# Kernel optimization log

Measured on AMD Instinct MI355X. Metric: run time of the kernel, lower is better.

## Reference

```python
import jax, jax.numpy as jnp
import numpy as np

DIM, HEADS, NB_FEATURES = 512, 8, 64
HEAD_DIM = DIM // HEADS


def setup_inputs() -> dict:
    key = jax.random.key(0)
    k_x, k_qkv, k_pm, k_wp, k_bp = jax.random.split(key, 5)
    B, N = 8, 4096
    x = jax.random.normal(k_x, (B, N, DIM), dtype=jnp.float32)
    # to_qkv: Linear(dim, 3*dim, bias=False) -> apply as x @ w_qkv
    w_qkv = jax.random.normal(k_qkv, (DIM, 3 * DIM), dtype=jnp.float32) * (1.0 / np.sqrt(DIM))
    # random projection buffer [H, D, F]
    proj_mat = jax.random.normal(k_pm, (HEADS, HEAD_DIM, NB_FEATURES), dtype=jnp.float32)
    # output projection Linear(dim, dim) with bias
    w_proj = jax.random.normal(k_wp, (DIM, DIM), dtype=jnp.float32) * (1.0 / np.sqrt(DIM))
    b_proj = jax.random.normal(k_bp, (DIM,), dtype=jnp.float32) * 0.01
    return {"x": x, "w_qkv": w_qkv, "proj_mat": proj_mat, "w_proj": w_proj, "b_proj": b_proj}


def _phi(t, proj_mat):
    # t: [B,N,H,D], proj_mat: [H,D,F] -> [B,N,H,F]
    return jax.nn.elu(jnp.einsum('bnhd,hdf->bnhf', t, proj_mat)) + 1.0


def reference(x, w_qkv, proj_mat, w_proj, b_proj):
    B, N, dim = x.shape
    H, D = HEADS, dim // HEADS
    qkv = x @ w_qkv  # [B,N,3*dim]
    q, k, v = jnp.split(qkv, 3, axis=-1)
    q = q.reshape(B, N, H, D)
    k = k.reshape(B, N, H, D)
    v = v.reshape(B, N, H, D)
    q_phi = _phi(q, proj_mat)  # [B,N,H,F]
    k_phi = _phi(k, proj_mat)  # [B,N,H,F]
    kv = jnp.einsum('bnhf,bnhd->bhfd', k_phi, v)  # [B,H,F,D]
    z = 1.0 / jnp.einsum('bnhf,bhf->bnh', q_phi, k_phi.sum(axis=1))  # [B,N,H]
    out = jnp.einsum('bnhf,bhfd,bnh->bnhd', q_phi, kv, z)  # [B,N,H,D]
    out = out.reshape(B, N, H * D)
    return out @ w_proj + b_proj
```

## Files before the change

### kernel.cpp

```cpp
#include <hip/hip_runtime.h>
#include <hip/hip_bf16.h>

typedef __bf16 bf16_t;
typedef __bf16 bf16x4 __attribute__((ext_vector_type(4)));
typedef __bf16 bf16x8 __attribute__((ext_vector_type(8)));
typedef float f32x4 __attribute__((ext_vector_type(4)));

__device__ __forceinline__ void gload16(const void* g, void* l) {
  __builtin_amdgcn_global_load_lds((const __attribute__((address_space(1))) void*)g,
                                   (__attribute__((address_space(3))) void*)l, 16, 0, 0);
}

#define VMW(n) asm volatile("s_waitcnt vmcnt(" #n ")" ::: "memory")

__global__ __launch_bounds__(256) void prep_qk(const float* __restrict__ w_qkv,
                                               const float* __restrict__ proj,
                                               bf16_t* __restrict__ WeffT) {
  const int half = blockIdx.x >> 3, h = blockIdx.x & 7;
  const int i0 = blockIdx.y * 64;
  __shared__ float P[64 * 64];
  __shared__ float Wt[64][65];
  const int t = threadIdx.x;
  #pragma unroll
  for (int r = 0; r < 16; ++r) P[t + 256 * r] = proj[(size_t)h * 4096 + t + 256 * r];
  #pragma unroll
  for (int r = 0; r < 16; ++r) {
    const int idx = t + 256 * r;
    Wt[idx >> 6][idx & 63] =
        w_qkv[(size_t)(i0 + (idx >> 6)) * 1536 + half * 512 + h * 64 + (idx & 63)];
  }
  __syncthreads();
  const int i = t & 63, fg = t >> 6;
  for (int f = fg; f < 64; f += 4) {
    float s = 0.f;
    #pragma unroll
    for (int d = 0; d < 64; ++d) s += Wt[i][d] * P[d * 64 + f];
    WeffT[(size_t)(half * 512 + h * 64 + f) * 512 + i0 + i] = (bf16_t)s;
  }
}

__global__ __launch_bounds__(256) void prep_v(const float* __restrict__ w_qkv,
                                              bf16_t* __restrict__ WeffT) {
  __shared__ bf16_t tile[32][33];
  const int i0 = blockIdx.x * 32, n0 = blockIdx.y * 32;
  const int tn = threadIdx.x & 31, ti = threadIdx.x >> 5;
  #pragma unroll
  for (int p = 0; p < 4; ++p) {
    const int i = ti + p * 8;
    tile[i][tn] = (bf16_t)w_qkv[(size_t)(i0 + i) * 1536 + 1024 + n0 + tn];
  }
  __syncthreads();
  #pragma unroll
  for (int p = 0; p < 4; ++p) {
    const int n = ti + p * 8;
    WeffT[(size_t)(1024 + n0 + n) * 512 + i0 + tn] = tile[tn][n];
  }
}

__global__ __launch_bounds__(256) void cast_x(const f32x4* __restrict__ x,
                                              bf16x4* __restrict__ xb, int n4) {
  int i = blockIdx.x * 256 + threadIdx.x;
  if (i < n4) {
    f32x4 v = x[i];
    bf16x4 o;
    #pragma unroll
    for (int j = 0; j < 4; ++j) o[j] = (bf16_t)v[j];
    xb[i] = o;
  }
}

__global__ __launch_bounds__(512, 2) void gemm_qkv8(const bf16_t* __restrict__ x_bf,
                                                    const bf16_t* __restrict__ WeffT,
                                                    bf16_t* __restrict__ q_phi,
                                                    bf16_t* __restrict__ kT,
                                                    bf16_t* __restrict__ vT) {
  __shared__ alignas(16) char smem[131072];
  const int t = threadIdx.x;
  const int wid = t >> 6, l = t & 63;
  const int wr = wid >> 2, wc = wid & 3;
  const int lrow = l & 15, lkb = l >> 4;
  const int hw = blockIdx.x;
  const int bid = (hw & 7) * 96 + (hw >> 3);
  const int tb = bid / 6, fb = bid % 6;
  const size_t tok0 = (size_t)tb * 256;
  const int f0 = fb * 256;
  const bf16_t* Ap = x_bf + tok0 * 512;
  const bf16_t* Bp = WeffT + (size_t)f0 * 512;

  const int sr = t >> 2, su = t & 3;
  const int f_sr = (sr >> 1) & 3;
  const size_t a_off0 = (size_t)sr * 512 + ((su ^ f_sr) * 8);
  const size_t a_off1 = (size_t)(sr + 128) * 512 + ((su ^ f_sr) * 8);

  auto stageA = [&](int s) {
    char* dst = smem + (s & 3) * 16384;
    gload16(Ap + a_off0 + s * 32, dst + t * 16);
    gload16(Ap + a_off1 + s * 32, dst + 8192 + t * 16);
  };
  auto stageB = [&](int s) {
    char* dst = smem + 65536 + (s & 3) * 16384;
    gload16(Bp + a_off0 + s * 32, dst + t * 16);
    gload16(Bp + a_off1 + s * 32, dst + 8192 + t * 16);
  };

  int woff[8], xoff[4];
  #pragma unroll
  for (int m = 0; m < 8; ++m) {
    const int r = wr * 128 + m * 16 + lrow;
    woff[m] = r * 64 + ((lkb ^ ((r >> 1) & 3)) << 4);
  }
  #pragma unroll
  for (int n = 0; n < 4; ++n) {
    const int r = wc * 64 + n * 16 + lrow;
    xoff[n] = r * 64 + ((lkb ^ ((r >> 1) & 3)) << 4);
  }

  f32x4 acc[8][4];
  #pragma unroll
  for (int m = 0; m < 8; ++m)
    #pragma unroll
    for (int n = 0; n < 4; ++n) acc[m][n] = f32x4{0.f, 0.f, 0.f, 0.f};

  stageA(0); stageB(0); stageA(1); stageB(1); stageA(2); stageB(2);
  VMW(8);
  __builtin_amdgcn_s_barrier();

  #pragma unroll
  for (int kt = 0; kt < 16; ++kt) {
    const char* Xs = smem + (kt & 3) * 16384;
    const char* Ws = smem + 65536 + (kt & 3) * 16384;
    bf16x8 wf[4], xf[4];
    #pragma unroll
    for (int m = 0; m < 4; ++m) wf[m] = *(const bf16x8*)(Ws + woff[m]);
    #pragma unroll
    for (int n = 0; n < 4; ++n) xf[n] = *(const bf16x8*)(Xs + xoff[n]);
    if (kt + 3 < 16) stageA(kt + 3);
    __builtin_amdgcn_s_setprio(1);
    #pragma unroll
    for (int m = 0; m < 4; ++m)
      #pragma unroll
      for (int n = 0; n < 4; ++n)
        acc[m][n] = __builtin_amdgcn_mfma_f32_16x16x32_bf16(wf[m], xf[n], acc[m][n], 0, 0, 0);
    __builtin_amdgcn_s_setprio(0);
    #pragma unroll
    for (int m = 0; m < 4; ++m) wf[m] = *(const bf16x8*)(Ws + woff[4 + m]);
    if (kt + 3 < 16) stageB(kt + 3);
    __builtin_amdgcn_s_setprio(1);
    #pragma unroll
    for (int m = 0; m < 4; ++m)
      #pragma unroll
      for (int n = 0; n < 4; ++n)
        acc[4 + m][n] = __builtin_amdgcn_mfma_f32_16x16x32_bf16(wf[m], xf[n], acc[4 + m][n], 0, 0, 0);
    __builtin_amdgcn_s_setprio(0);
    if (kt <= 12) { VMW(8); } else if (kt == 13) { VMW(4); } else if (kt == 14) { VMW(0); }
    __builtin_amdgcn_s_barrier();
  }

  const bool doElu = (fb < 4);
  #pragma unroll
  for (int m = 0; m < 8; ++m) {
    const int feat = wr * 128 + m * 16 + lkb * 4;
    const int ub = feat >> 3, bo = (feat & 7) * 2;
    #pragma unroll
    for (int n = 0; n < 4; ++n) {
      const int trow = wc * 64 + n * 16 + lrow;
      bf16x4 o;
      #pragma unroll
      for (int j = 0; j < 4; ++j) {
        float v = acc[m][n][j];
        if (doElu) v = v > 0.f ? v + 1.f : __expf(v);
        o[j] = (bf16_t)v;
      }
      const int s = (trow ^ (trow >> 3)) & 7;
      *(bf16x4*)(smem + trow * 512 + ((ub ^ s) << 4) + bo) = o;
    }
  }
  __syncthreads();
  if (fb < 2) {
    #pragma unroll
    for (int p = 0; p < 16; ++p) {
      const int flat = p * 512 + t;
      const int trow = flat >> 5, u = flat & 31;
      const int s = (trow ^ (trow >> 3)) & 7;
      bf16x8 vv = *(const bf16x8*)(smem + trow * 512 + ((u ^ s) << 4));
      *(bf16x8*)&q_phi[(tok0 + trow) * 512 + f0 + u * 8] = vv;
    }
  } else {
    const int b = (int)(tok0 >> 12);
    const int nn0 = (int)(tok0 & 4095);
    bf16_t* base = (fb < 4) ? (kT + ((size_t)(b * 512 + (fb - 2) * 256)) * 4096)
                            : (vT + ((size_t)(b * 512 + (fb - 4) * 256)) * 4096);
    #pragma unroll
    for (int p = 0; p < 16; ++p) {
      const int fl = (p & 7) * 32 + (t >> 4);
      const int tg = (p >> 3) * 16 + (t & 15);
      const int ub = fl >> 3, bo = (fl & 7) * 2;
      bf16x8 vv;
      #pragma unroll
      for (int j = 0; j < 8; ++j) {
        const int tok = tg * 8 + j;
        const int s = (tok ^ (tok >> 3)) & 7;
        vv[j] = *(const bf16_t*)(smem + tok * 512 + ((ub ^ s) << 4) + bo);
      }
      *(bf16x8*)(base + (size_t)fl * 4096 + nn0 + tg * 8) = vv;
    }
  }
}

__global__ __launch_bounds__(256) void kv_mfma(const bf16_t* __restrict__ kT,
                                               const bf16_t* __restrict__ vT,
                                               float* __restrict__ kv,
                                               float* __restrict__ ksum) {
  const int bh = blockIdx.x;
  const int nbase = blockIdx.y * 512;
  __shared__ alignas(16) char smem[32768];
  const int t = threadIdx.x, w = t >> 6, l = t & 63;
  const int wr = w >> 1, wc = w & 1;
  const int lrow = l & 15, lkb = l >> 4;
  const int st_r = l >> 3;
  const int st_c = ((l & 7) ^ st_r) * 8;
  const bf16_t* Kp = kT + (size_t)bh * 64 * 4096;
  const bf16_t* Vp = vT + (size_t)bh * 64 * 4096;

  f32x4 acc[2][2];
  #pragma unroll
  for (int m = 0; m < 2; ++m)
    #pragma unroll
    for (int n = 0; n < 2; ++n) acc[m][n] = f32x4{0.f, 0.f, 0.f, 0.f};
  float ksf[2] = {0.f, 0.f};

  #pragma unroll
  for (int c = 0; c < 2; ++c) {
    const int q8 = w * 2 + c;
    gload16(Kp + (size_t)(q8 * 8 + st_r) * 4096 + nbase + st_c, smem + q8 * 1024);
    gload16(Vp + (size_t)(q8 * 8 + st_r) * 4096 + nbase + st_c, smem + 8192 + q8 * 1024);
  }
  __syncthreads();

  int cur = 0;
  for (int st = 0; st < 8; ++st) {
    if (st < 7) {
      char* nb = smem + (cur ^ 1) * 16384;
      const int nb2 = nbase + (st + 1) * 64;
      #pragma unroll
      for (int c = 0; c < 2; ++c) {
        const int q8 = w * 2 + c;
        gload16(Kp + (size_t)(q8 * 8 + st_r) * 4096 + nb2 + st_c, nb + q8 * 1024);
        gload16(Vp + (size_t)(q8 * 8 + st_r) * 4096 + nb2 + st_c, nb + 8192 + q8 * 1024);
      }
    }
    const char* KsB = smem + cur * 16384;
    const char* VsB = KsB + 8192;
    bf16x8 af[2][2], bf[2][2];
    #pragma unroll
    for (int m = 0; m < 2; ++m) {
      const int r = wr * 32 + m * 16 + lrow;
      #pragma unroll
      for (int kk = 0; kk < 2; ++kk) {
        const int kb = lkb + kk * 4;
        af[m][kk] = *(const bf16x8*)(KsB + r * 128 + (((kb ^ (r & 7)) & 7) << 4));
      }
    }
    #pragma unroll
    for (int n = 0; n < 2; ++n) {
      const int r = wc * 32 + n * 16 + lrow;
      #pragma unroll
      for (int kk = 0; kk < 2; ++kk) {
        const int kb = lkb + kk * 4;
        bf[n][kk] = *(const bf16x8*)(VsB + r * 128 + (((kb ^ (r & 7)) & 7) << 4));
      }
    }
    #pragma unroll
    for (int m = 0; m < 2; ++m)
      #pragma unroll
      for (int n = 0; n < 2; ++n) {
        acc[m][n] = __builtin_amdgcn_mfma_f32_16x16x32_bf16(af[m][0], bf[n][0], acc[m][n], 0, 0, 0);
        acc[m][n] = __builtin_amdgcn_mfma_f32_16x16x32_bf16(af[m][1], bf[n][1], acc[m][n], 0, 0, 0);
      }
    if (wc == 0) {
      #pragma unroll
      for (int m = 0; m < 2; ++m)
        #pragma unroll
        for (int kk = 0; kk < 2; ++kk)
          #pragma unroll
          for (int j = 0; j < 8; ++j) ksf[m] += (float)af[m][kk][j];
    }
    __syncthreads();
    cur ^= 1;
  }

  float* kvp = kv + (size_t)bh * 4096;
  #pragma unroll
  for (int m = 0; m < 2; ++m)
    #pragma unroll
    for (int n = 0; n < 2; ++n)
      #pragma unroll
      for (int j = 0; j < 4; ++j)
        atomicAdd(&kvp[(wr * 32 + m * 16 + lkb * 4 + j) * 64 + wc * 32 + n * 16 + lrow],
                  acc[m][n][j]);
  if (wc == 0) {
    #pragma unroll
    for (int m = 0; m < 2; ++m) {
      float s = ksf[m];
      s += __shfl_xor(s, 16);
      s += __shfl_xor(s, 32);
      if (l < 16) atomicAdd(&ksum[(size_t)bh * 64 + wr * 32 + m * 16 + l], s);
    }
  }
}

__global__ __launch_bounds__(256) void w2_kernel(const float* __restrict__ kv,
                                                 const float* __restrict__ w_proj,
                                                 bf16_t* __restrict__ W2T) {
  const int bh = blockIdx.x, b = bh >> 3, h = bh & 7;
  const int j0 = blockIdx.y * 64;
  const int t = threadIdx.x;
  __shared__ float kvs[64][64];
  __shared__ float wps[64][64];
  const float* kvp = kv + (size_t)bh * 4096;
  #pragma unroll
  for (int i = 0; i < 16; ++i) ((float*)kvs)[t + 256 * i] = kvp[t + 256 * i];
  {
    const int d = t >> 2, c16 = (t & 3) * 16;
    const float* src = w_proj + (size_t)(h * 64 + d) * 512 + j0 + c16;
    #pragma unroll
    for (int j = 0; j < 16; ++j) wps[d][c16 + j] = src[j];
  }
  __syncthreads();
  const int fq = t >> 4, jq = t & 15;
  float acc[4][4] = {};
  for (int d = 0; d < 64; ++d) {
    float kf[4], wj[4];
    #pragma unroll
    for (int i = 0; i < 4; ++i) kf[i] = kvs[fq * 4 + i][d];
    #pragma unroll
    for (int i = 0; i < 4; ++i) wj[i] = wps[d][jq * 4 + i];
    #pragma unroll
    for (int i = 0; i < 4; ++i)
      #pragma unroll
      for (int j = 0; j < 4; ++j) acc[i][j] += kf[i] * wj[j];
  }
  #pragma unroll
  for (int j = 0; j < 4; ++j)
    #pragma unroll
    for (int i = 0; i < 4; ++i)
      W2T[((size_t)b * 512 + j0 + jq * 4 + j) * 512 + h * 64 + fq * 4 + i] = (bf16_t)acc[i][j];
}

__global__ __launch_bounds__(256) void zq_kernel(const bf16_t* __restrict__ qphi,
                                                 const float* __restrict__ ksum,
                                                 bf16_t* __restrict__ zq) {
  const int row = blockIdx.x * 4 + (threadIdx.x >> 6);
  const int l = threadIdx.x & 63;
  const int b = row >> 12;
  const int h = l >> 3, f8 = (l & 7) * 8;
  const bf16_t* src = qphi + (size_t)row * 512 + h * 64 + f8;
  bf16x8 v = *(const bf16x8*)src;
  const float* ks = ksum + ((size_t)b * 8 + h) * 64 + f8;
  float part = 0.f;
  float vf[8];
  #pragma unroll
  for (int j = 0; j < 8; ++j) { vf[j] = (float)v[j]; part += vf[j] * ks[j]; }
  part += __shfl_xor(part, 1);
  part += __shfl_xor(part, 2);
  part += __shfl_xor(part, 4);
  const float z = 1.f / part;
  bf16x8 o;
  #pragma unroll
  for (int j = 0; j < 8; ++j) o[j] = (bf16_t)(vf[j] * z);
  *(bf16x8*)(zq + (size_t)row * 512 + h * 64 + f8) = o;
}

__global__ __launch_bounds__(256) void gemm_out(const bf16_t* __restrict__ W2T,
                                                const bf16_t* __restrict__ zq,
                                                float* __restrict__ Cout,
                                                const float* __restrict__ bias) {
  constexpr int K = 512, BK = 64;
  __shared__ alignas(16) char smem[65536];
  const int t = threadIdx.x, w = t >> 6, l = t & 63;
  const int hw = blockIdx.x;
  const int bid = (hw & 7) * 128 + (hw >> 3);
  const int z = bid >> 7;
  const int rem = bid & 127;
  const int qblk = rem >> 2, pblk = rem & 3;
  const size_t tok0 = (size_t)qblk * 128;
  const int pj0 = pblk * 128;
  const bf16_t* Pp = W2T + ((size_t)z * 512 + pj0) * 512;
  const bf16_t* Qp = zq + ((size_t)z * 4096 + tok0) * 512;

  const int wr = w >> 1, wc = w & 1;
  const int lrow = l & 15, lkb = l >> 4;
  const int st_r = l >> 3;
  const int st_c = ((l & 7) ^ st_r) * 8;

  f32x4 acc[4][4];
  #pragma unroll
  for (int m = 0; m < 4; ++m)
    #pragma unroll
    for (int n = 0; n < 4; ++n) acc[m][n] = f32x4{0.f, 0.f, 0.f, 0.f};

  #pragma unroll
  for (int c = 0; c < 4; ++c) {
    const int q8 = c * 4 + w;
    gload16(Pp + (size_t)(q8 * 8 + st_r) * K + st_c, smem + q8 * 1024);
    gload16(Qp + (size_t)(q8 * 8 + st_r) * K + st_c, smem + 16384 + q8 * 1024);
  }
  __syncthreads();

  int cur = 0;
  for (int kt = 0; kt < K; kt += BK) {
    if (kt + BK < K) {
      char* nb = smem + (cur ^ 1) * 32768;
      #pragma unroll
      for (int c = 0; c < 4; ++c) {
        const int q8 = c * 4 + w;
        gload16(Pp + (size_t)(q8 * 8 + st_r) * K + kt + BK + st_c, nb + q8 * 1024);
        gload16(Qp + (size_t)(q8 * 8 + st_r) * K + kt + BK + st_c, nb + 16384 + q8 * 1024);
      }
    }
    const char* PsB = smem + cur * 32768;
    const char* QsB = PsB + 16384;
    bf16x8 pf[4][2], qf[4][2];
    #pragma unroll
    for (int m = 0; m < 4; ++m) {
      const int r = wr * 64 + m * 16 + lrow;
      #pragma unroll
      for (int kk = 0; kk < 2; ++kk) {
        const int kb = lkb + kk * 4;
        pf[m][kk] = *(const bf16x8*)(PsB + r * 128 + (((kb ^ (r & 7)) & 7) << 4));
      }
    }
    #pragma unroll
    for (int n = 0; n < 4; ++n) {
      const int r = wc * 64 + n * 16 + lrow;
      #pragma unroll
      for (int kk = 0; kk < 2; ++kk) {
        const int kb = lkb + kk * 4;
        qf[n][kk] = *(const bf16x8*)(QsB + r * 128 + (((kb ^ (r & 7)) & 7) << 4));
      }
    }
    #pragma unroll
    for (int m = 0; m < 4; ++m)
      #pragma unroll
      for (int n = 0; n < 4; ++n) {
        acc[m][n] = __builtin_amdgcn_mfma_f32_16x16x32_bf16(pf[m][0], qf[n][0], acc[m][n], 0, 0, 0);
        acc[m][n] = __builtin_amdgcn_mfma_f32_16x16x32_bf16(pf[m][1], qf[n][1], acc[m][n], 0, 0, 0);
      }
    __syncthreads();
    cur ^= 1;
  }

  float* ep = (float*)smem;
  #pragma unroll
  for (int p = 0; p < 2; ++p) {
    if (p) __syncthreads();
    #pragma unroll
    for (int nn2 = 0; nn2 < 2; ++nn2) {
      const int n = p * 2 + nn2;
      const int r6 = wc * 32 + (n & 1) * 16 + lrow;
      #pragma unroll
      for (int m = 0; m < 4; ++m) {
        const int pr0 = wr * 64 + m * 16 + lkb * 4;
        f32x4 v = acc[m][n];
        const f32x4 bv = *(const f32x4*)&bias[pj0 + pr0];
        #pragma unroll
        for (int j = 0; j < 4; ++j) v[j] += bv[j];
        const int u = pr0 >> 2;
        *(f32x4*)((char*)ep + r6 * 512 + ((u ^ (r6 & 31)) << 4)) = v;
      }
    }
    __syncthreads();
    #pragma unroll
    for (int i = 0; i < 8; ++i) {
      const int flat = i * 256 + t;
      const int r6 = flat >> 5, u2 = flat & 31;
      f32x4 v = *(const f32x4*)((char*)ep + r6 * 512 + ((u2 ^ (r6 & 31)) << 4));
      const int qc = (r6 >> 5) * 64 + p * 32 + (r6 & 31);
      *(f32x4*)&Cout[((size_t)z * 4096 + tok0 + qc) * 512 + pj0 + u2 * 4] = v;
    }
  }
}

extern "C" void kernel_launch(void* const* d_in, const int* in_sizes, int n_in,
                              void* d_out, int out_size, void* d_ws, size_t ws_size,
                              hipStream_t stream) {
  const float* x      = (const float*)d_in[0];
  const float* w_qkv  = (const float*)d_in[1];
  const float* proj   = (const float*)d_in[2];
  const float* w_proj = (const float*)d_in[3];
  const float* b_proj = (const float*)d_in[4];
  float* out = (float*)d_out;
  char* ws = (char*)d_ws;

  bf16_t* x_bf  = (bf16_t*)(ws + 0);
  bf16_t* WeffT = (bf16_t*)(ws + 33554432);
  bf16_t* q_phi = (bf16_t*)(ws + 35127296);
  bf16_t* kT    = (bf16_t*)(ws + 68681728);
  bf16_t* vT    = (bf16_t*)(ws + 102236160);
  float*  kv    = (float*)(ws + 135790592);
  float*  ksum  = (float*)(ws + 136839168);
  bf16_t* W2T   = (bf16_t*)(ws + 136855552);
  bf16_t* zq    = (bf16_t*)(ws + 141049856);

  prep_qk<<<dim3(16, 8), 256, 0, stream>>>(w_qkv, proj, WeffT);
  prep_v<<<dim3(16, 16), 256, 0, stream>>>(w_qkv, WeffT);
  cast_x<<<16384, 256, 0, stream>>>((const f32x4*)x, (bf16x4*)x_bf, 4194304);
  gemm_qkv8<<<768, 512, 0, stream>>>(x_bf, WeffT, q_phi, kT, vT);
  hipMemsetAsync(kv, 0, 1048576 + 16384, stream);
  kv_mfma<<<dim3(64, 8), 256, 0, stream>>>(kT, vT, kv, ksum);
  w2_kernel<<<dim3(64, 8), 256, 0, stream>>>(kv, w_proj, W2T);
  zq_kernel<<<8192, 256, 0, stream>>>(q_phi, ksum, zq);
  gemm_out<<<1024, 256, 0, stream>>>(W2T, zq, out, b_proj);
}
```

Baseline: 184.8 us.

## Fuse x cast into QKV GEMM and z-normalization into output GEMM

Removes the standalone cast_x and zq_kernel launches. The QKV GEMM now reads fp32 x directly, converting it to bf16 in registers before writing to LDS. The output GEMM loads q_phi, computes the per-head normalizer from ksum held in LDS, and writes the scaled bf16 tile into LDS itself. This drops the intermediate x_bf and zq round-trips through HBM. In exchange, the A-operand pipeline shrinks to register prefetch with double buffering, B uses triple buffering, LDS drops to 80KB, and the epilogue is split into two halves.

```diff
diff --git a/kernel.cpp b/kernel.cpp
--- a/kernel.cpp
+++ b/kernel.cpp
@@ -4,6 +4,7 @@
 typedef __bf16 bf16_t;
 typedef __bf16 bf16x4 __attribute__((ext_vector_type(4)));
 typedef __bf16 bf16x8 __attribute__((ext_vector_type(8)));
+typedef float f32x2 __attribute__((ext_vector_type(2)));
 typedef float f32x4 __attribute__((ext_vector_type(4)));
 
 __device__ __forceinline__ void gload16(const void* g, void* l) {
@@ -12,6 +13,7 @@
 }
 
 #define VMW(n) asm volatile("s_waitcnt vmcnt(" #n ")" ::: "memory")
+#define LGKM0() asm volatile("s_waitcnt lgkmcnt(0)" ::: "memory")
 
 __global__ __launch_bounds__(256) void prep_qk(const float* __restrict__ w_qkv,
                                                const float* __restrict__ proj,
@@ -57,24 +59,12 @@
   }
 }
 
-__global__ __launch_bounds__(256) void cast_x(const f32x4* __restrict__ x,
-                                              bf16x4* __restrict__ xb, int n4) {
-  int i = blockIdx.x * 256 + threadIdx.x;
-  if (i < n4) {
-    f32x4 v = x[i];
-    bf16x4 o;
-    #pragma unroll
-    for (int j = 0; j < 4; ++j) o[j] = (bf16_t)v[j];
-    xb[i] = o;
-  }
-}
-
-__global__ __launch_bounds__(512, 2) void gemm_qkv8(const bf16_t* __restrict__ x_bf,
+__global__ __launch_bounds__(512, 2) void gemm_qkv8(const float* __restrict__ x,
                                                     const bf16_t* __restrict__ WeffT,
                                                     bf16_t* __restrict__ q_phi,
                                                     bf16_t* __restrict__ kT,
                                                     bf16_t* __restrict__ vT) {
-  __shared__ alignas(16) char smem[131072];
+  __shared__ alignas(16) char smem[81920];
   const int t = threadIdx.x;
   const int wid = t >> 6, l = t & 63;
   const int wr = wid >> 2, wc = wid & 3;
@@ -84,23 +74,37 @@
   const int tb = bid / 6, fb = bid % 6;
   const size_t tok0 = (size_t)tb * 256;
   const int f0 = fb * 256;
-  const bf16_t* Ap = x_bf + tok0 * 512;
+  const float* Ap = x + tok0 * 512;
   const bf16_t* Bp = WeffT + (size_t)f0 * 512;
 
   const int sr = t >> 2, su = t & 3;
   const int f_sr = (sr >> 1) & 3;
-  const size_t a_off0 = (size_t)sr * 512 + ((su ^ f_sr) * 8);
-  const size_t a_off1 = (size_t)(sr + 128) * 512 + ((su ^ f_sr) * 8);
-
-  auto stageA = [&](int s) {
-    char* dst = smem + (s & 3) * 16384;
-    gload16(Ap + a_off0 + s * 32, dst + t * 16);
-    gload16(Ap + a_off1 + s * 32, dst + 8192 + t * 16);
+  const int scol = (su ^ f_sr) * 8;
+
+  f32x4 areg[4];
+  auto loadA = [&](int s) {
+    const float* p0 = Ap + (size_t)sr * 512 + scol + s * 32;
+    const float* p1 = Ap + (size_t)(sr + 128) * 512 + scol + s * 32;
+    areg[0] = *(const f32x4*)p0;
+    areg[1] = *(const f32x4*)(p0 + 4);
+    areg[2] = *(const f32x4*)p1;
+    areg[3] = *(const f32x4*)(p1 + 4);
+  };
+  auto writeA = [&](int s) {
+    char* dst = smem + (s & 1) * 16384;
+    bf16x8 o0, o1;
+    #pragma unroll
+    for (int j = 0; j < 4; ++j) {
+      o0[j] = (bf16_t)areg[0][j]; o0[4 + j] = (bf16_t)areg[1][j];
+      o1[j] = (bf16_t)areg[2][j]; o1[4 + j] = (bf16_t)areg[3][j];
+    }
+    *(bf16x8*)(dst + t * 16) = o0;
+    *(bf16x8*)(dst + 8192 + t * 16) = o1;
   };
   auto stageB = [&](int s) {
-    char* dst = smem + 65536 + (s & 3) * 16384;
-    gload16(Bp + a_off0 + s * 32, dst + t * 16);
-    gload16(Bp + a_off1 + s * 32, dst + 8192 + t * 16);
+    char* dst = smem + 32768 + (s % 3) * 16384;
+    gload16(Bp + (size_t)sr * 512 + scol + s * 32, dst + t * 16);
+    gload16(Bp + (size_t)(sr + 128) * 512 + scol + s * 32, dst + 8192 + t * 16);
   };
 
   int woff[8], xoff[4];
@@ -121,20 +125,23 @@
     #pragma unroll
     for (int n = 0; n < 4; ++n) acc[m][n] = f32x4{0.f, 0.f, 0.f, 0.f};
 
-  stageA(0); stageB(0); stageA(1); stageB(1); stageA(2); stageB(2);
-  VMW(8);
+  loadA(0); stageB(0); stageB(1);
+  writeA(0);
+  VMW(2);
+  LGKM0();
   __builtin_amdgcn_s_barrier();
 
   #pragma unroll
   for (int kt = 0; kt < 16; ++kt) {
-    const char* Xs = smem + (kt & 3) * 16384;
-    const char* Ws = smem + 65536 + (kt & 3) * 16384;
+    const char* Xs = smem + (kt & 1) * 16384;
+    const char* Ws = smem + 32768 + (kt % 3) * 16384;
     bf16x8 wf[4], xf[4];
     #pragma unroll
     for (int m = 0; m < 4; ++m) wf[m] = *(const bf16x8*)(Ws + woff[m]);
     #pragma unroll
     for (int n = 0; n < 4; ++n) xf[n] = *(const bf16x8*)(Xs + xoff[n]);
-    if (kt + 3 < 16) stageA(kt + 3);
+    if (kt + 1 < 16) loadA(kt + 1);
+    if (kt + 2 < 16) stageB(kt + 2);
     __builtin_amdgcn_s_setprio(1);
     #pragma unroll
     for (int m = 0; m < 4; ++m)
@@ -144,7 +151,6 @@
     __builtin_amdgcn_s_setprio(0);
     #pragma unroll
     for (int m = 0; m < 4; ++m) wf[m] = *(const bf16x8*)(Ws + woff[4 + m]);
-    if (kt + 3 < 16) stageB(kt + 3);
     __builtin_amdgcn_s_setprio(1);
     #pragma unroll
     for (int m = 0; m < 4; ++m)
@@ -152,57 +158,65 @@
       for (int n = 0; n < 4; ++n)
         acc[4 + m][n] = __builtin_amdgcn_mfma_f32_16x16x32_bf16(wf[m], xf[n], acc[4 + m][n], 0, 0, 0);
     __builtin_amdgcn_s_setprio(0);
-    if (kt <= 12) { VMW(8); } else if (kt == 13) { VMW(4); } else if (kt == 14) { VMW(0); }
+    if (kt + 1 < 16) writeA(kt + 1);
+    if (kt <= 13) { VMW(2); } else if (kt == 14) { VMW(0); }
+    LGKM0();
     __builtin_amdgcn_s_barrier();
   }
 
   const bool doElu = (fb < 4);
-  #pragma unroll
-  for (int m = 0; m < 8; ++m) {
-    const int feat = wr * 128 + m * 16 + lkb * 4;
-    const int ub = feat >> 3, bo = (feat & 7) * 2;
-    #pragma unroll
-    for (int n = 0; n < 4; ++n) {
-      const int trow = wc * 64 + n * 16 + lrow;
-      bf16x4 o;
-      #pragma unroll
-      for (int j = 0; j < 4; ++j) {
-        float v = acc[m][n][j];
-        if (doElu) v = v > 0.f ? v + 1.f : __expf(v);
-        o[j] = (bf16_t)v;
-      }
-      const int s = (trow ^ (trow >> 3)) & 7;
-      *(bf16x4*)(smem + trow * 512 + ((ub ^ s) << 4) + bo) = o;
-    }
-  }
-  __syncthreads();
-  if (fb < 2) {
-    #pragma unroll
-    for (int p = 0; p < 16; ++p) {
-      const int flat = p * 512 + t;
-      const int trow = flat >> 5, u = flat & 31;
-      const int s = (trow ^ (trow >> 3)) & 7;
-      bf16x8 vv = *(const bf16x8*)(smem + trow * 512 + ((u ^ s) << 4));
-      *(bf16x8*)&q_phi[(tok0 + trow) * 512 + f0 + u * 8] = vv;
-    }
-  } else {
-    const int b = (int)(tok0 >> 12);
-    const int nn0 = (int)(tok0 & 4095);
-    bf16_t* base = (fb < 4) ? (kT + ((size_t)(b * 512 + (fb - 2) * 256)) * 4096)
-                            : (vT + ((size_t)(b * 512 + (fb - 4) * 256)) * 4096);
-    #pragma unroll
-    for (int p = 0; p < 16; ++p) {
-      const int fl = (p & 7) * 32 + (t >> 4);
-      const int tg = (p >> 3) * 16 + (t & 15);
-      const int ub = fl >> 3, bo = (fl & 7) * 2;
-      bf16x8 vv;
-      #pragma unroll
-      for (int j = 0; j < 8; ++j) {
-        const int tok = tg * 8 + j;
-        const int s = (tok ^ (tok >> 3)) & 7;
-        vv[j] = *(const bf16_t*)(smem + tok * 512 + ((ub ^ s) << 4) + bo);
-      }
-      *(bf16x8*)(base + (size_t)fl * 4096 + nn0 + tg * 8) = vv;
+  const int b = (int)(tok0 >> 12);
+  const int nn0 = (int)(tok0 & 4095);
+  #pragma unroll
+  for (int p = 0; p < 2; ++p) {
+    if (p) __syncthreads();
+    if ((wc >> 1) == p) {
+      #pragma unroll
+      for (int m = 0; m < 8; ++m) {
+        const int feat = wr * 128 + m * 16 + lkb * 4;
+        const int ub = feat >> 3, bo = (feat & 7) * 2;
+        #pragma unroll
+        for (int n = 0; n < 4; ++n) {
+          const int trow = (wc & 1) * 64 + n * 16 + lrow;
+          bf16x4 o;
+          #pragma unroll
+          for (int j = 0; j < 4; ++j) {
+            float v = acc[m][n][j];
+            if (doElu) v = v > 0.f ? v + 1.f : __expf(v);
+            o[j] = (bf16_t)v;
+          }
+          const int s = (trow ^ (trow >> 3)) & 7;
+          *(bf16x4*)(smem + trow * 512 + ((ub ^ s) << 4) + bo) = o;
+        }
+      }
+    }
+    __syncthreads();
+    if (fb < 2) {
+      #pragma unroll
+      for (int i = 0; i < 8; ++i) {
+        const int flat = i * 512 + t;
+        const int trow = flat >> 5, u = flat & 31;
+        const int s = (trow ^ (trow >> 3)) & 7;
+        bf16x8 vv = *(const bf16x8*)(smem + trow * 512 + ((u ^ s) << 4));
+        *(bf16x8*)&q_phi[(tok0 + p * 128 + trow) * 512 + f0 + u * 8] = vv;
+      }
+    } else {
+      bf16_t* base = (fb < 4) ? (kT + ((size_t)(b * 512 + (fb - 2) * 256)) * 4096)
+                              : (vT + ((size_t)(b * 512 + (fb - 4) * 256)) * 4096);
+      #pragma unroll
+      for (int i = 0; i < 8; ++i) {
+        const int flat = i * 512 + t;
+        const int fl = flat >> 4, tg = flat & 15;
+        const int ub = fl >> 3, bo = (fl & 7) * 2;
+        bf16x8 vv;
+        #pragma unroll
+        for (int j = 0; j < 8; ++j) {
+          const int tok = tg * 8 + j;
+          const int s = (tok ^ (tok >> 3)) & 7;
+          vv[j] = *(const bf16_t*)(smem + tok * 512 + ((ub ^ s) << 4) + bo);
+        }
+        *(bf16x8*)(base + (size_t)fl * 4096 + nn0 + p * 128 + tg * 8) = vv;
+      }
     }
   }
 }
@@ -347,36 +361,12 @@
       W2T[((size_t)b * 512 + j0 + jq * 4 + j) * 512 + h * 64 + fq * 4 + i] = (bf16_t)acc[i][j];
 }
 
-__global__ __launch_bounds__(256) void zq_kernel(const bf16_t* __restrict__ qphi,
-                                                 const float* __restrict__ ksum,
-                                                 bf16_t* __restrict__ zq) {
-  const int row = blockIdx.x * 4 + (threadIdx.x >> 6);
-  const int l = threadIdx.x & 63;
-  const int b = row >> 12;
-  const int h = l >> 3, f8 = (l & 7) * 8;
-  const bf16_t* src = qphi + (size_t)row * 512 + h * 64 + f8;
-  bf16x8 v = *(const bf16x8*)src;
-  const float* ks = ksum + ((size_t)b * 8 + h) * 64 + f8;
-  float part = 0.f;
-  float vf[8];
-  #pragma unroll
-  for (int j = 0; j < 8; ++j) { vf[j] = (float)v[j]; part += vf[j] * ks[j]; }
-  part += __shfl_xor(part, 1);
-  part += __shfl_xor(part, 2);
-  part += __shfl_xor(part, 4);
-  const float z = 1.f / part;
-  bf16x8 o;
-  #pragma unroll
-  for (int j = 0; j < 8; ++j) o[j] = (bf16_t)(vf[j] * z);
-  *(bf16x8*)(zq + (size_t)row * 512 + h * 64 + f8) = o;
-}
-
 __global__ __launch_bounds__(256) void gemm_out(const bf16_t* __restrict__ W2T,
-                                                const bf16_t* __restrict__ zq,
+                                                const bf16_t* __restrict__ q_phi,
+                                                const float* __restrict__ ksum,
                                                 float* __restrict__ Cout,
                                                 const float* __restrict__ bias) {
-  constexpr int K = 512, BK = 64;
-  __shared__ alignas(16) char smem[65536];
+  __shared__ alignas(16) char smem[67584];
   const int t = threadIdx.x, w = t >> 6, l = t & 63;
   const int hw = blockIdx.x;
   const int bid = (hw & 7) * 128 + (hw >> 3);
@@ -386,12 +376,67 @@
   const size_t tok0 = (size_t)qblk * 128;
   const int pj0 = pblk * 128;
   const bf16_t* Pp = W2T + ((size_t)z * 512 + pj0) * 512;
-  const bf16_t* Qp = zq + ((size_t)z * 4096 + tok0) * 512;
 
   const int wr = w >> 1, wc = w & 1;
   const int lrow = l & 15, lkb = l >> 4;
   const int st_r = l >> 3;
   const int st_c = ((l & 7) ^ st_r) * 8;
+  const int token = t >> 1, half = t & 1;
+  float* ks_lds = (float*)(smem + 65536);
+
+  bf16x8 breg[4];
+  auto loadB = [&](int c) {
+    const bf16_t* p = q_phi + ((size_t)z * 4096 + tok0 + token) * 512 + c * 64 + half * 32;
+    breg[0] = *(const bf16x8*)p;
+    breg[1] = *(const bf16x8*)(p + 8);
+    breg[2] = *(const bf16x8*)(p + 16);
+    breg[3] = *(const bf16x8*)(p + 24);
+  };
+  auto stageA = [&](int s) {
+    #pragma unroll
+    for (int c = 0; c < 4; ++c) {
+      const int q8 = c * 4 + w;
+      gload16(Pp + (size_t)(q8 * 8 + st_r) * 512 + s * 64 + st_c,
+              smem + (s & 1) * 16384 + q8 * 1024);
+    }
+  };
+  auto procB = [&](int c) {
+    const f32x4* ksv = (const f32x4*)(ks_lds + c * 64 + half * 32);
+    float vals[32];
+    float dot = 0.f;
+    #pragma unroll
+    for (int g = 0; g < 8; ++g) {
+      const f32x4 kk = ksv[g];
+      #pragma unroll
+      for (int j = 0; j < 4; ++j) {
+        const float v = (float)breg[g >> 1][(g & 1) * 4 + j];
+        vals[g * 4 + j] = v;
+        dot += v * kk[j];
+      }
+    }
+    dot += __shfl_xor(dot, 1);
+    const float zz = 1.f / dot;
+    char* dst = smem + 32768 + (c & 1) * 16384;
+    #pragma unroll
+    for (int g = 0; g < 4; ++g) {
+      bf16x8 o;
+      #pragma unroll
+      for (int j = 0; j < 8; ++j) o[j] = (bf16_t)(vals[g * 8 + j] * zz);
+      const int uk = half * 4 + g;
+      *(bf16x8*)(dst + token * 128 + ((uk ^ (token & 7)) << 4)) = o;
+    }
+  };
+
+  {
+    const f32x2 kk = *(const f32x2*)&ksum[(size_t)z * 512 + t * 2];
+    *(f32x2*)&ks_lds[t * 2] = kk;
+  }
+  __syncthreads();
+  loadB(0);
+  stageA(0);
+  procB(0);
+  VMW(0);
+  __syncthreads();
 
   f32x4 acc[4][4];
   #pragma unroll
@@ -399,27 +444,9 @@
     #pragma unroll
     for (int n = 0; n < 4; ++n) acc[m][n] = f32x4{0.f, 0.f, 0.f, 0.f};
 
-  #pragma unroll
-  for (int c = 0; c < 4; ++c) {
-    const int q8 = c * 4 + w;
-    gload16(Pp + (size_t)(q8 * 8 + st_r) * K + st_c, smem + q8 * 1024);
-    gload16(Qp + (size_t)(q8 * 8 + st_r) * K + st_c, smem + 16384 + q8 * 1024);
-  }
-  __syncthreads();
-
-  int cur = 0;
-  for (int kt = 0; kt < K; kt += BK) {
-    if (kt + BK < K) {
-      char* nb = smem + (cur ^ 1) * 32768;
-      #pragma unroll
-      for (int c = 0; c < 4; ++c) {
-        const int q8 = c * 4 + w;
-        gload16(Pp + (size_t)(q8 * 8 + st_r) * K + kt + BK + st_c, nb + q8 * 1024);
-        gload16(Qp + (size_t)(q8 * 8 + st_r) * K + kt + BK + st_c, nb + 16384 + q8 * 1024);
-      }
-    }
-    const char* PsB = smem + cur * 32768;
-    const char* QsB = PsB + 16384;
+  for (int kt = 0; kt < 8; ++kt) {
+    const char* PsB = smem + (kt & 1) * 16384;
+    const char* QsB = smem + 32768 + (kt & 1) * 16384;
     bf16x8 pf[4][2], qf[4][2];
     #pragma unroll
     for (int m = 0; m < 4; ++m) {
@@ -439,6 +466,7 @@
         qf[n][kk] = *(const bf16x8*)(QsB + r * 128 + (((kb ^ (r & 7)) & 7) << 4));
       }
     }
+    if (kt + 1 < 8) { loadB(kt + 1); stageA(kt + 1); }
     #pragma unroll
     for (int m = 0; m < 4; ++m)
       #pragma unroll
@@ -446,8 +474,8 @@
         acc[m][n] = __builtin_amdgcn_mfma_f32_16x16x32_bf16(pf[m][0], qf[n][0], acc[m][n], 0, 0, 0);
         acc[m][n] = __builtin_amdgcn_mfma_f32_16x16x32_bf16(pf[m][1], qf[n][1], acc[m][n], 0, 0, 0);
       }
+    if (kt + 1 < 8) { procB(kt + 1); VMW(0); }
     __syncthreads();
-    cur ^= 1;
   }
 
   float* ep = (float*)smem;
@@ -492,23 +520,19 @@
   float* out = (float*)d_out;
   char* ws = (char*)d_ws;
 
-  bf16_t* x_bf  = (bf16_t*)(ws + 0);
-  bf16_t* WeffT = (bf16_t*)(ws + 33554432);
-  bf16_t* q_phi = (bf16_t*)(ws + 35127296);
-  bf16_t* kT    = (bf16_t*)(ws + 68681728);
-  bf16_t* vT    = (bf16_t*)(ws + 102236160);
-  float*  kv    = (float*)(ws + 135790592);
-  float*  ksum  = (float*)(ws + 136839168);
-  bf16_t* W2T   = (bf16_t*)(ws + 136855552);
-  bf16_t* zq    = (bf16_t*)(ws + 141049856);
+  bf16_t* WeffT = (bf16_t*)(ws + 0);
+  bf16_t* q_phi = (bf16_t*)(ws + 1572864);
+  bf16_t* kT    = (bf16_t*)(ws + 35127296);
+  bf16_t* vT    = (bf16_t*)(ws + 68681728);
+  float*  kv    = (float*)(ws + 102236160);
+  float*  ksum  = (float*)(ws + 103284736);
+  bf16_t* W2T   = (bf16_t*)(ws + 103301120);
 
   prep_qk<<<dim3(16, 8), 256, 0, stream>>>(w_qkv, proj, WeffT);
   prep_v<<<dim3(16, 16), 256, 0, stream>>>(w_qkv, WeffT);
-  cast_x<<<16384, 256, 0, stream>>>((const f32x4*)x, (bf16x4*)x_bf, 4194304);
-  gemm_qkv8<<<768, 512, 0, stream>>>(x_bf, WeffT, q_phi, kT, vT);
+  gemm_qkv8<<<768, 512, 0, stream>>>(x, WeffT, q_phi, kT, vT);
   hipMemsetAsync(kv, 0, 1048576 + 16384, stream);
   kv_mfma<<<dim3(64, 8), 256, 0, stream>>>(kT, vT, kv, ksum);
   w2_kernel<<<dim3(64, 8), 256, 0, stream>>>(kv, w_proj, W2T);
-  zq_kernel<<<8192, 256, 0, stream>>>(q_phi, ksum, zq);
-  gemm_out<<<1024, 256, 0, stream>>>(W2T, zq, out, b_proj);
-}
+  gemm_out<<<1024, 256, 0, stream>>>(W2T, q_phi, ksum, out, b_proj);
+}
```

New measurement: 177.1 us. 1.04x faster.
